# Kernel tuning notes

Hardware: AMD Instinct MI355X
Metric: run time of the kernel (lower is better)

Reference implementation:

```python
import jax, jax.numpy as jnp
import numpy as np

B = 4_000_000

# physical constants from initBatteryParams
R_ = 8.3144621
F_ = 96487.0
ALPHA = 0.5
SN = 0.0002
SP = 0.0002
KN = 20000.0
KP = 20000.0
VOL = 2.2e-05
VOLS = 0.1 * VOL
VOLB = VOL - VOLS
TO = 10.0
TSN = 90.0
TSP = 90.0
U0P = 4.03
U0N = 0.01
QMAX_BASE = 10000.0
RO_BASE = 10.0
T_DIFFUSION = 7.0e6  # repo default; attribute used in getNextState
DT = 1.0


def setup_inputs() -> dict:
    key = jax.random.key(0)
    ks = jax.random.split(key, 12)
    qMax = 1.4 * jnp.ones((B,), jnp.float32)   # 14000/qMaxBASE
    Ro = 0.015 * jnp.ones((B,), jnp.float32)   # 0.15/RoBASE
    # physically plausible initial state (get_initial_state) + small noise
    qM = qMax * QMAX_BASE  # [B]
    Tb = 292.1 + 0.5 * jax.random.normal(ks[0], (B, 1), jnp.float32)
    Vo = 0.01 * jax.random.uniform(ks[1], (B, 1), jnp.float32)
    Vsn = 0.01 * jax.random.uniform(ks[2], (B, 1), jnp.float32)
    Vsp = 0.01 * jax.random.uniform(ks[3], (B, 1), jnp.float32)
    jitter = lambda k: 1.0 + 0.01 * jax.random.normal(k, (B, 1), jnp.float32)
    qnB = (qM * 0.6 * VOLB / VOL)[:, None] * jitter(ks[4])
    qnS = (qM * 0.6 * VOLS / VOL)[:, None] * jitter(ks[5])
    qpB = (qM * 0.4 * VOLB / VOL)[:, None] * jitter(ks[6])
    qpS = (qM * 0.4 * VOLS / VOL)[:, None] * jitter(ks[7])
    states = jnp.concatenate([Tb, Vo, Vsn, Vsp, qnB, qnS, qpB, qpS], axis=1)
    inputs = 1.0 + 2.0 * jax.random.uniform(ks[8], (B, 1), jnp.float32)  # current [A]
    kw = jax.random.split(ks[9], 8)
    return {
        "inputs": inputs, "states": states, "qMax": qMax, "Ro": Ro,
        "Wp0": 0.5 * jax.random.normal(kw[0], (8, 1), jnp.float32),
        "bp0": 0.1 * jax.random.normal(kw[1], (8,), jnp.float32),
        "Wp2": 0.5 * jax.random.normal(kw[2], (4, 8), jnp.float32),
        "bp2": 0.1 * jax.random.normal(kw[3], (4,), jnp.float32),
        "Wp4": 0.5 * jax.random.normal(kw[4], (1, 4), jnp.float32),
        "bp4": 0.1 * jax.random.normal(kw[5], (1,), jnp.float32),
        "Wn": 0.0016 * jnp.ones((1, 1), jnp.float32),  # ~fitted Linear(1,1)
        "bn": -0.0008 * jnp.ones((1,), jnp.float32),
    }


def _mlp_p(x, Wp0, bp0, Wp2, bp2, Wp4, bp4):
    h = jnp.tanh(x @ Wp0.T + bp0)
    h = jnp.tanh(h @ Wp2.T + bp2)
    return h @ Wp4.T + bp4


def _cell(inputs, states, qMax, Ro, Wp0, bp0, Wp2, bp2, Wp4, bp4, Wn, bn):
    Tb, Vo, Vsn, Vsp, qnB, qnS, qpB, qpS = jnp.split(states, 8, axis=1)
    i = inputs  # [B,1]
    qSMax = (qMax * QMAX_BASE * VOLS / VOL)[:, None]  # [B,1]
    # --- getNextState ---
    xpS = jnp.clip(qpS / qSMax, 1e-18, 1.0)
    xnS = jnp.clip(qnS / qSMax, 1e-18, 1.0)
    Jn0 = 1e-18 + KN * (1.0 - xnS) ** ALPHA * xnS ** ALPHA
    Jp0 = 1e-18 + KP * (1.0 - xpS) ** ALPHA * xpS ** ALPHA
    qdotDiffusionBSn = (qnB / VOLB - qnS / VOLS) / T_DIFFUSION
    qdotDiffusionBSp = (qpB / VOLB - qpS / VOLS) / T_DIFFUSION
    Jn = i / SN
    Jp = i / SP
    VoNominal = i * Ro[:, None] * RO_BASE
    VsnNominal = R_ * Tb / F_ / ALPHA * jnp.arcsinh(Jn / (2.0 * Jn0))
    VspNominal = R_ * Tb / F_ / ALPHA * jnp.arcsinh(Jp / (2.0 * Jp0))
    Tb2 = Tb  # Tbdot = 0
    Vo2 = Vo + (VoNominal - Vo) / TO * DT
    Vsn2 = Vsn + (VsnNominal - Vsn) / TSN * DT
    Vsp2 = Vsp + (VspNominal - Vsp) / TSP * DT
    qnB2 = qnB + (-qdotDiffusionBSn) * DT
    qnS2 = qnS + (qdotDiffusionBSn - i) * DT
    qpB2 = qpB + (-qdotDiffusionBSp) * DT
    qpS2 = qpS + (i + qdotDiffusionBSp) * DT
    XNew = jnp.concatenate([Tb2, Vo2, Vsn2, Vsp2, qnB2, qnS2, qpB2, qpS2], axis=1)
    # --- getNextOutput (on XNew) ---
    xpS_o = qpS2 / qSMax
    xnS_o = qnS2 / qSMax
    VepMLP = _mlp_p(xpS_o, Wp0, bp0, Wp2, bp2, Wp4, bp4)
    VenMLP = xnS_o @ Wn.T + bn
    safe_log_p = jnp.clip((1.0 - xpS_o) / xpS_o, 1e-18, 1e18)
    safe_log_n = jnp.clip((1.0 - xnS_o) / xnS_o, 1e-18, 1e18)
    Vep = U0P + R_ * Tb2 / F_ * jnp.log(safe_log_p) + VepMLP
    Ven = U0N + R_ * Tb2 / F_ * jnp.log(safe_log_n) + VenMLP
    V = Vep - Ven - Vo2 - Vsn2 - Vsp2
    return V, XNew


def reference(inputs, states, qMax, Ro, Wp0, bp0, Wp2, bp2, Wp4, bp4, Wn, bn):
    return _cell(inputs, states, qMax, Ro, Wp0, bp0, Wp2, bp2, Wp4, bp4, Wn, bn)
```

## Files before the change

### kernel.cpp

```cpp
#include <hip/hip_runtime.h>

__device__ __forceinline__ float fdiv_fast(float a, float b) {
    return __fdividef(a, b);
}

__device__ __forceinline__ float tanh_fast(float x) {
    float t = fminf(fmaxf(2.0f * x, -80.0f), 80.0f);
    float e = __expf(t);
    return fdiv_fast(e - 1.0f, e + 1.0f);
}

__device__ __forceinline__ float asinh_pos(float x) {
    return __logf(x + sqrtf(fmaf(x, x, 1.0f)));
}

#define RTF     (8.3144621f / 96487.0f)
#define VOL_    2.2e-05f
#define VOLS_   2.2e-06f
#define VOLB_   1.98e-05f
#define INV_TDIFF (1.0f / 7.0e6f)

__global__ __launch_bounds__(256) void battery_cell_kernel(
    const float* __restrict__ inp,
    const float* __restrict__ st,
    const float* __restrict__ qMaxp,
    const float* __restrict__ Rop,
    const float* __restrict__ Wp0,
    const float* __restrict__ bp0,
    const float* __restrict__ Wp2,
    const float* __restrict__ bp2,
    const float* __restrict__ Wp4,
    const float* __restrict__ bp4,
    const float* __restrict__ Wn,
    const float* __restrict__ bn,
    float* __restrict__ outV,
    float* __restrict__ outX,
    int B)
{
    int b = blockIdx.x * blockDim.x + threadIdx.x;
    if (b >= B) return;

    const float4* st4 = (const float4*)st;
    float4 s0 = st4[2 * b];
    float4 s1 = st4[2 * b + 1];
    float Tb  = s0.x, Vo  = s0.y, Vsn = s0.z, Vsp = s0.w;
    float qnB = s1.x, qnS = s1.y, qpB = s1.z, qpS = s1.w;
    float i   = inp[b];
    float qm  = qMaxp[b];
    float ro  = Rop[b];

    float w0[8], b0v[8], w2v[32], b2v[4], w4v[4];
#pragma unroll
    for (int j = 0; j < 8; j++) { w0[j] = Wp0[j]; b0v[j] = bp0[j]; }
#pragma unroll
    for (int j = 0; j < 32; j++) w2v[j] = Wp2[j];
#pragma unroll
    for (int j = 0; j < 4; j++)  { b2v[j] = bp2[j]; w4v[j] = Wp4[j]; }
    float wb4 = bp4[0], wn = Wn[0], wbn = bn[0];

    float qSMax = qm * 1000.0f;
    float invq  = fdiv_fast(1.0f, qSMax);

    float xpS = fminf(fmaxf(qpS * invq, 1e-18f), 1.0f);
    float xnS = fminf(fmaxf(qnS * invq, 1e-18f), 1.0f);
    float Jn0 = 1e-18f + 20000.0f * sqrtf((1.0f - xnS) * xnS);
    float Jp0 = 1e-18f + 20000.0f * sqrtf((1.0f - xpS) * xpS);

    float qdotn = (qnB * (1.0f / VOLB_) - qnS * (1.0f / VOLS_)) * INV_TDIFF;
    float qdotp = (qpB * (1.0f / VOLB_) - qpS * (1.0f / VOLS_)) * INV_TDIFF;

    float Jn = i * 5000.0f;
    float Jp = i * 5000.0f;
    float VoNom  = i * ro * 10.0f;
    float coef   = RTF * Tb * 2.0f;
    float VsnNom = coef * asinh_pos(fdiv_fast(Jn, 2.0f * Jn0));
    float VspNom = coef * asinh_pos(fdiv_fast(Jp, 2.0f * Jp0));

    float Vo2  = Vo  + (VoNom  - Vo ) * 0.1f;
    float Vsn2 = Vsn + (VsnNom - Vsn) * (1.0f / 90.0f);
    float Vsp2 = Vsp + (VspNom - Vsp) * (1.0f / 90.0f);
    float qnB2 = qnB - qdotn;
    float qnS2 = qnS + qdotn - i;
    float qpB2 = qpB - qdotp;
    float qpS2 = qpS + i + qdotp;

    float xp = qpS2 * invq;
    float xn = qnS2 * invq;

    float h1[8];
#pragma unroll
    for (int j = 0; j < 8; j++)
        h1[j] = tanh_fast(fmaf(xp, w0[j], b0v[j]));
    float vep_mlp = wb4;
#pragma unroll
    for (int k = 0; k < 4; k++) {
        float a = b2v[k];
#pragma unroll
        for (int j = 0; j < 8; j++)
            a = fmaf(h1[j], w2v[k * 8 + j], a);
        vep_mlp = fmaf(tanh_fast(a), w4v[k], vep_mlp);
    }
    float ven_mlp = fmaf(xn, wn, wbn);

    float rp = fminf(fmaxf(fdiv_fast(1.0f - xp, xp), 1e-18f), 1e18f);
    float rn = fminf(fmaxf(fdiv_fast(1.0f - xn, xn), 1e-18f), 1e18f);
    float rtb = RTF * Tb;
    float Vep = 4.03f + rtb * __logf(rp) + vep_mlp;
    float Ven = 0.01f + rtb * __logf(rn) + ven_mlp;
    float V = Vep - Ven - Vo2 - Vsn2 - Vsp2;

    outV[b] = V;
    float4 o0 = make_float4(Tb, Vo2, Vsn2, Vsp2);
    float4 o1 = make_float4(qnB2, qnS2, qpB2, qpS2);
    float4* ox4 = (float4*)outX;
    ox4[2 * b]     = o0;
    ox4[2 * b + 1] = o1;
}

extern "C" void kernel_launch(void* const* d_in, const int* in_sizes, int n_in,
                              void* d_out, int out_size, void* d_ws, size_t ws_size,
                              hipStream_t stream) {
    const float* inp  = (const float*)d_in[0];
    const float* st   = (const float*)d_in[1];
    const float* qMax = (const float*)d_in[2];
    const float* Ro   = (const float*)d_in[3];
    const float* Wp0  = (const float*)d_in[4];
    const float* bp0  = (const float*)d_in[5];
    const float* Wp2  = (const float*)d_in[6];
    const float* bp2  = (const float*)d_in[7];
    const float* Wp4  = (const float*)d_in[8];
    const float* bp4  = (const float*)d_in[9];
    const float* Wn   = (const float*)d_in[10];
    const float* bn   = (const float*)d_in[11];

    int B = in_sizes[0];
    float* outV = (float*)d_out;
    float* outX = (float*)d_out + B;

    int block = 256;
    int grid = (B + block - 1) / block;
    battery_cell_kernel<<<grid, block, 0, stream>>>(
        inp, st, qMax, Ro, Wp0, bp0, Wp2, bp2, Wp4, bp4, Wn, bn,
        outV, outX, B);
}
```

Measured before the change: 286.9 us.

## Replace per-element MLP, log and sqrt with interpolated lookup tables

A small pre-kernel evaluates the P-side MLP, the RT/F·log((1-x)/x) term and 1/(2·Jn0) on a 4096-point grid over [0,1]; it runs every call from the current weights. The main kernel then replaces 12 tanh evaluations, two sqrt, two log and several divisions per element with linear interpolation of gathered table entries. This is meant to remove the transcendental-heavy ALU work that likely dominates the kernel. In exchange it adds a second launch, scattered table reads, and interpolation error, especially near x=0 or 1 where sqrt and log are steep.

Measured after the change: 286.9 us. Within noise of the previous version (-0.0%).

```diff
diff --git a/kernel.cpp b/kernel.cpp
--- a/kernel.cpp
+++ b/kernel.cpp
@@ -1,38 +1,67 @@
 #include <hip/hip_runtime.h>
+#include <math.h>
+
+typedef float v4f __attribute__((ext_vector_type(4)));
+typedef float v2f __attribute__((ext_vector_type(2)));
+
+#define RTF       (8.3144621f / 96487.0f)
+#define VOLS_     2.2e-06f
+#define VOLB_     1.98e-05f
+#define INV_TDIFF (1.0f / 7.0e6f)
+
+#define LUT_N 4096
 
 __device__ __forceinline__ float fdiv_fast(float a, float b) {
     return __fdividef(a, b);
-}
-
-__device__ __forceinline__ float tanh_fast(float x) {
-    float t = fminf(fmaxf(2.0f * x, -80.0f), 80.0f);
-    float e = __expf(t);
-    return fdiv_fast(e - 1.0f, e + 1.0f);
 }
 
 __device__ __forceinline__ float asinh_pos(float x) {
     return __logf(x + sqrtf(fmaf(x, x, 1.0f)));
 }
 
-#define RTF     (8.3144621f / 96487.0f)
-#define VOL_    2.2e-05f
-#define VOLS_   2.2e-06f
-#define VOLB_   1.98e-05f
-#define INV_TDIFF (1.0f / 7.0e6f)
+__global__ __launch_bounds__(256) void build_lut_kernel(
+    const float* __restrict__ Wp0, const float* __restrict__ bp0,
+    const float* __restrict__ Wp2, const float* __restrict__ bp2,
+    const float* __restrict__ Wp4, const float* __restrict__ bp4,
+    float* __restrict__ lutJ, v2f* __restrict__ lutO)
+{
+    int idx = blockIdx.x * blockDim.x + threadIdx.x;
+    if (idx >= LUT_N) return;
+    float x = (float)idx * (1.0f / (float)(LUT_N - 1));
+
+    float j0 = 1e-18f + 20000.0f * sqrtf(fmaxf(x * (1.0f - x), 0.0f));
+    lutJ[idx] = 1.0f / (2.0f * j0);
+
+    float h1[8];
+#pragma unroll
+    for (int j = 0; j < 8; j++)
+        h1[j] = tanhf(fmaf(x, Wp0[j], bp0[j]));
+    float mlp = bp4[0];
+#pragma unroll
+    for (int k = 0; k < 4; k++) {
+        float a = bp2[k];
+#pragma unroll
+        for (int j = 0; j < 8; j++)
+            a = fmaf(h1[j], Wp2[k * 8 + j], a);
+        mlp = fmaf(tanhf(a), Wp4[k], mlp);
+    }
+
+    float r = fminf(fmaxf((1.0f - x) / fmaxf(x, 1e-30f), 1e-18f), 1e18f);
+    float lg = RTF * logf(r);
+
+    v2f o; o.x = mlp; o.y = lg;
+    lutO[idx] = o;
+}
 
 __global__ __launch_bounds__(256) void battery_cell_kernel(
     const float* __restrict__ inp,
     const float* __restrict__ st,
     const float* __restrict__ qMaxp,
     const float* __restrict__ Rop,
-    const float* __restrict__ Wp0,
-    const float* __restrict__ bp0,
-    const float* __restrict__ Wp2,
-    const float* __restrict__ bp2,
-    const float* __restrict__ Wp4,
-    const float* __restrict__ bp4,
     const float* __restrict__ Wn,
     const float* __restrict__ bn,
+    const float* __restrict__ lutJ,
+    const v2f*   __restrict__ lutO,
     float* __restrict__ outV,
     float* __restrict__ outX,
     int B)
@@ -40,41 +69,40 @@
     int b = blockIdx.x * blockDim.x + threadIdx.x;
     if (b >= B) return;
 
-    const float4* st4 = (const float4*)st;
-    float4 s0 = st4[2 * b];
-    float4 s1 = st4[2 * b + 1];
+    const v4f* st4 = (const v4f*)st;
+    v4f s0 = st4[2 * b];
+    v4f s1 = st4[2 * b + 1];
     float Tb  = s0.x, Vo  = s0.y, Vsn = s0.z, Vsp = s0.w;
     float qnB = s1.x, qnS = s1.y, qpB = s1.z, qpS = s1.w;
     float i   = inp[b];
     float qm  = qMaxp[b];
     float ro  = Rop[b];
+    float wn  = Wn[0], wbn = bn[0];
 
-    float w0[8], b0v[8], w2v[32], b2v[4], w4v[4];
-#pragma unroll
-    for (int j = 0; j < 8; j++) { w0[j] = Wp0[j]; b0v[j] = bp0[j]; }
-#pragma unroll
-    for (int j = 0; j < 32; j++) w2v[j] = Wp2[j];
-#pragma unroll
-    for (int j = 0; j < 4; j++)  { b2v[j] = bp2[j]; w4v[j] = Wp4[j]; }
-    float wb4 = bp4[0], wn = Wn[0], wbn = bn[0];
-
-    float qSMax = qm * 1000.0f;
-    float invq  = fdiv_fast(1.0f, qSMax);
+    float invq = fdiv_fast(1.0f, qm * 1000.0f);
 
     float xpS = fminf(fmaxf(qpS * invq, 1e-18f), 1.0f);
     float xnS = fminf(fmaxf(qnS * invq, 1e-18f), 1.0f);
-    float Jn0 = 1e-18f + 20000.0f * sqrtf((1.0f - xnS) * xnS);
-    float Jp0 = 1e-18f + 20000.0f * sqrtf((1.0f - xpS) * xpS);
+
+    float tn = xnS * (float)(LUT_N - 1);
+    float tp = xpS * (float)(LUT_N - 1);
+    int in0 = min((int)tn, LUT_N - 2);
+    int ip0 = min((int)tp, LUT_N - 2);
+    float fn = tn - (float)in0;
+    float fp = tp - (float)ip0;
+    float jn_a = lutJ[in0], jn_b = lutJ[in0 + 1];
+    float jp_a = lutJ[ip0], jp_b = lutJ[ip0 + 1];
+    float inv2Jn = fmaf(fn, jn_b - jn_a, jn_a);
+    float inv2Jp = fmaf(fp, jp_b - jp_a, jp_a);
 
     float qdotn = (qnB * (1.0f / VOLB_) - qnS * (1.0f / VOLS_)) * INV_TDIFF;
     float qdotp = (qpB * (1.0f / VOLB_) - qpS * (1.0f / VOLS_)) * INV_TDIFF;
 
     float Jn = i * 5000.0f;
-    float Jp = i * 5000.0f;
     float VoNom  = i * ro * 10.0f;
     float coef   = RTF * Tb * 2.0f;
-    float VsnNom = coef * asinh_pos(fdiv_fast(Jn, 2.0f * Jn0));
-    float VspNom = coef * asinh_pos(fdiv_fast(Jp, 2.0f * Jp0));
+    float VsnNom = coef * asinh_pos(Jn * inv2Jn);
+    float VspNom = coef * asinh_pos(Jn * inv2Jp);
 
     float Vo2  = Vo  + (VoNom  - Vo ) * 0.1f;
     float Vsn2 = Vsn + (VsnNom - Vsn) * (1.0f / 90.0f);
@@ -87,32 +115,26 @@
     float xp = qpS2 * invq;
     float xn = qnS2 * invq;
 
-    float h1[8];
-#pragma unroll
-    for (int j = 0; j < 8; j++)
-        h1[j] = tanh_fast(fmaf(xp, w0[j], b0v[j]));
-    float vep_mlp = wb4;
-#pragma unroll
-    for (int k = 0; k < 4; k++) {
-        float a = b2v[k];
-#pragma unroll
-        for (int j = 0; j < 8; j++)
-            a = fmaf(h1[j], w2v[k * 8 + j], a);
-        vep_mlp = fmaf(tanh_fast(a), w4v[k], vep_mlp);
-    }
-    float ven_mlp = fmaf(xn, wn, wbn);
+    float tpo = fminf(fmaxf(xp, 0.0f), 1.0f) * (float)(LUT_N - 1);
+    float tno = fminf(fmaxf(xn, 0.0f), 1.0f) * (float)(LUT_N - 1);
+    int ipo = min((int)tpo, LUT_N - 2);
+    int ino = min((int)tno, LUT_N - 2);
+    float fpo = tpo - (float)ipo;
+    float fno = tno - (float)ino;
+    v2f oa = lutO[ipo], ob = lutO[ipo + 1];
+    v2f na = lutO[ino], nb = lutO[ino + 1];
+    float mlp_p = fmaf(fpo, ob.x - oa.x, oa.x);
+    float log_p = fmaf(fpo, ob.y - oa.y, oa.y);
+    float log_n = fmaf(fno, nb.y - na.y, na.y);
 
-    float rp = fminf(fmaxf(fdiv_fast(1.0f - xp, xp), 1e-18f), 1e18f);
-    float rn = fminf(fmaxf(fdiv_fast(1.0f - xn, xn), 1e-18f), 1e18f);
-    float rtb = RTF * Tb;
-    float Vep = 4.03f + rtb * __logf(rp) + vep_mlp;
-    float Ven = 0.01f + rtb * __logf(rn) + ven_mlp;
+    float Vep = 4.03f + Tb * log_p + mlp_p;
+    float Ven = 0.01f + Tb * log_n + fmaf(xn, wn, wbn);
     float V = Vep - Ven - Vo2 - Vsn2 - Vsp2;
 
     outV[b] = V;
-    float4 o0 = make_float4(Tb, Vo2, Vsn2, Vsp2);
-    float4 o1 = make_float4(qnB2, qnS2, qpB2, qpS2);
-    float4* ox4 = (float4*)outX;
+    v4f o0; o0.x = Tb;   o0.y = Vo2;  o0.z = Vsn2; o0.w = Vsp2;
+    v4f o1; o1.x = qnB2; o1.y = qnS2; o1.z = qpB2; o1.w = qpS2;
+    v4f* ox4 = (v4f*)outX;
     ox4[2 * b]     = o0;
     ox4[2 * b + 1] = o1;
 }
@@ -137,9 +159,14 @@
     float* outV = (float*)d_out;
     float* outX = (float*)d_out + B;
 
+    float* lutJ = (float*)d_ws;
+    v2f*   lutO = (v2f*)((char*)d_ws + LUT_N * 4);
+
+    build_lut_kernel<<<LUT_N / 256, 256, 0, stream>>>(
+        Wp0, bp0, Wp2, bp2, Wp4, bp4, lutJ, lutO);
+
     int block = 256;
     int grid = (B + block - 1) / block;
     battery_cell_kernel<<<grid, block, 0, stream>>>(
-        inp, st, qMax, Ro, Wp0, bp0, Wp2, bp2, Wp4, bp4, Wn, bn,
-        outV, outX, B);
+        inp, st, qMax, Ro, Wn, bn, lutJ, lutO, outV, outX, B);
 }
```
